# Optimization experiments

Hardware: AMD Instinct MI355X
Metric: run time of the kernel (lower is better)

The kernel has to match this reference:

```python
import jax, jax.numpy as jnp
import numpy as np

HIDDEN = 1024
HEADS = 16
HEAD_DIM = HIDDEN // HEADS


def setup_inputs() -> dict:
    key = jax.random.key(0)
    k_x, k_wq, k_bq, k_wo, k_bo = jax.random.split(key, 5)
    x = jax.random.normal(k_x, (2, 2048, HIDDEN), dtype=jnp.float32)
    s = 1.0 / np.sqrt(HIDDEN)
    W_qkv = jax.random.uniform(k_wq, (HIDDEN, 3 * HIDDEN), jnp.float32, -s, s)
    b_qkv = jax.random.uniform(k_bq, (3 * HIDDEN,), jnp.float32, -s, s)
    W_out = jax.random.uniform(k_wo, (HIDDEN, HIDDEN), jnp.float32, -s, s)
    b_out = jax.random.uniform(k_bo, (HIDDEN,), jnp.float32, -s, s)
    return {"x": x, "W_qkv": W_qkv, "b_qkv": b_qkv, "W_out": W_out, "b_out": b_out}


def reference(x, W_qkv, b_qkv, W_out, b_out):
    B, S, D = x.shape
    qkv = x @ W_qkv + b_qkv                       # [B,S,3D]
    qkv = qkv.reshape(B, S, 3, HEADS, HEAD_DIM)
    qkv = jnp.transpose(qkv, (2, 0, 3, 1, 4))     # [3,B,H,S,Dh]
    q, k, v = qkv[0], qkv[1], qkv[2]
    scores = jnp.einsum("bhsd,bhtd->bhst", q, k) / np.sqrt(HEAD_DIM)
    attn = jax.nn.softmax(scores, axis=-1)        # [B,H,S,S]
    out = jnp.einsum("bhst,bhtd->bhsd", attn, v)  # [B,H,S,Dh]
    out = jnp.transpose(out, (0, 2, 1, 3)).reshape(B, S, D)
    return out @ W_out + b_out
```

## Files before the change

### kernel.cpp

```cpp
#include <hip/hip_runtime.h>
#include <hip/hip_bf16.h>

typedef short short8 __attribute__((ext_vector_type(8)));
typedef float float4_ __attribute__((ext_vector_type(4)));
typedef unsigned short ushort_t;
typedef unsigned int uint32_t_;
typedef uint32_t_ uint2v __attribute__((ext_vector_type(2)));
typedef uint32_t_ uint4v __attribute__((ext_vector_type(4)));

#define SCL 0.1803368801111f

__device__ __forceinline__ ushort_t f2bf(float f) {
    uint32_t_ u = __builtin_bit_cast(uint32_t_, f);
    u = (u + 0x7fffu + ((u >> 16) & 1u)) >> 16;
    return (ushort_t)u;
}

__device__ __forceinline__ uint32_t_ pack_bf16(float a, float b) {
    uint32_t_ ua = __builtin_bit_cast(uint32_t_, a) + 0x8000u;
    uint32_t_ ub = __builtin_bit_cast(uint32_t_, b) + 0x8000u;
    return __builtin_amdgcn_perm(ub, ua, 0x07060302);
}

__device__ __forceinline__ uint32_t_ cvt_pk_bf16(float lo, float hi) {
    uint32_t_ r;
    asm("v_cvt_pk_bf16_f32 %0, %1, %2" : "=v"(r) : "v"(lo), "v"(hi));
    return r;
}

#define MFMA32(a, b, c) __builtin_amdgcn_mfma_f32_16x16x32_bf16(a, b, c, 0, 0, 0)

#define GLD_LDS16(g, l) __builtin_amdgcn_global_load_lds( \
    (const __attribute__((address_space(1))) void*)(g),   \
    (__attribute__((address_space(3))) void*)(l), 16, 0, 0)

__global__ __launch_bounds__(256)
void prep_k(const float* __restrict__ x, ushort_t* __restrict__ x_bf,
            const float* __restrict__ Wqkv, ushort_t* __restrict__ WqkvT,
            const float* __restrict__ Wout, ushort_t* __restrict__ WoutT) {
    __shared__ float tile[32][33];
    const int id = blockIdx.x;
    const int tid = threadIdx.x;
    if (id < 4096) {
        int i = (id * 256 + tid) * 4;
        float4 v = *(const float4*)(x + i);
        uint32_t_ lo = (uint32_t_)f2bf(v.x) | ((uint32_t_)f2bf(v.y) << 16);
        uint32_t_ hi = (uint32_t_)f2bf(v.z) | ((uint32_t_)f2bf(v.w) << 16);
        *(uint2*)(x_bf + i) = make_uint2(lo, hi);
        return;
    }
    const float* in;
    ushort_t* out;
    int N, K, n0, k0;
    if (id < 7168) {
        int t = id - 4096;
        in = Wqkv; out = WqkvT; N = 3072; K = 1024;
        n0 = (t % 96) * 32; k0 = (t / 96) * 32;
    } else {
        int t = id - 7168;
        in = Wout; out = WoutT; N = 1024; K = 1024;
        n0 = (t & 31) * 32; k0 = (t >> 5) * 32;
    }
    int tx = tid & 31, ty = tid >> 5;
    #pragma unroll
    for (int i = 0; i < 32; i += 8)
        tile[ty + i][tx] = in[(size_t)(k0 + ty + i) * N + n0 + tx];
    __syncthreads();
    #pragma unroll
    for (int i = 0; i < 32; i += 8)
        out[(size_t)(n0 + ty + i) * K + k0 + tx] = f2bf(tile[tx][ty + i]);
}

template <int TN, bool QKV_EPI>
__global__ __launch_bounds__(256, TN == 128 ? 3 : 4)
void gemm_dbuf_k(const ushort_t* __restrict__ A, const ushort_t* __restrict__ Bt,
                 const float* __restrict__ bias, void* __restrict__ C,
                 ushort_t* __restrict__ Vt_out, int M, int N, int K) {
    constexpr int NB   = TN / 32;
    constexpr int SETB = 8192 + TN * 64;
    __shared__ char smem[2 * SETB];
    const int tid  = threadIdx.x;
    const int nwg = gridDim.x * gridDim.y;
    const int id  = blockIdx.y * gridDim.x + blockIdx.x;
    const int sid = (id & 7) * (nwg >> 3) + (id >> 3);
    const int m0  = (sid / gridDim.x) * 128;
    const int n0  = (sid % gridDim.x) * TN;
    const int w    = tid >> 6;
    const int lane = tid & 63;
    const int wm   = (w >> 1) * 64;
    const int wn   = (w & 1) * (TN / 2);
    const int quad = lane >> 4;
    const int l16  = lane & 15;

    const int sr = 16 * w + (lane >> 2);
    const int sc = ((lane & 3) ^ ((sr >> 1) & 3)) * 8;
    const ushort_t* ag0 = A  + (size_t)(m0 + sr) * K + sc;
    const ushort_t* ag1 = A  + (size_t)(m0 + sr + 64) * K + sc;
    const ushort_t* bg0 = Bt + (size_t)(n0 + sr) * K + sc;
    const ushort_t* bg1 = Bt + (size_t)(n0 + sr + 64) * K + sc;
    char* sA = smem + 1024 * w;
    char* sB = smem + 8192 + 1024 * w;

    int aoff[4], boff[NB];
    #pragma unroll
    for (int i = 0; i < 4; i++) {
        int row = wm + i * 16 + l16;
        aoff[i] = row * 64 + ((quad ^ ((row >> 1) & 3)) * 16);
    }
    #pragma unroll
    for (int i = 0; i < NB; i++) {
        int row = wn + i * 16 + l16;
        boff[i] = 8192 + row * 64 + ((quad ^ ((row >> 1) & 3)) * 16);
    }

    float4_ acc[4][NB] = {};
    const int NIT = K >> 5;

    GLD_LDS16(ag0, sA);
    GLD_LDS16(ag1, sA + 4096);
    GLD_LDS16(bg0, sB);
    if (TN == 128) GLD_LDS16(bg1, sB + 4096);

    for (int it = 0; it < NIT; ++it) {
        __syncthreads();
        if (it + 1 < NIT) {
            const int nk = (it + 1) * 32;
            char* dA = sA + ((it + 1) & 1) * SETB;
            char* dB = sB + ((it + 1) & 1) * SETB;
            GLD_LDS16(ag0 + nk, dA);
            GLD_LDS16(ag1 + nk, dA + 4096);
            GLD_LDS16(bg0 + nk, dB);
            if (TN == 128) GLD_LDS16(bg1 + nk, dB + 4096);
        }
        const char* base = smem + (it & 1) * SETB;
        short8 af[4], bf[NB];
        #pragma unroll
        for (int i = 0; i < 4; i++)  af[i] = *(const short8*)(base + aoff[i]);
        #pragma unroll
        for (int i = 0; i < NB; i++) bf[i] = *(const short8*)(base + boff[i]);
        #pragma unroll
        for (int mi = 0; mi < 4; mi++)
            #pragma unroll
            for (int ni = 0; ni < NB; ni++)
                acc[mi][ni] = MFMA32(af[mi], bf[ni], acc[mi][ni]);
    }

    #pragma unroll
    for (int mi = 0; mi < 4; mi++) {
        int row = m0 + wm + mi * 16 + quad * 4;
        #pragma unroll
        for (int ni = 0; ni < NB; ni++) {
            int col = n0 + wn + ni * 16 + l16;
            float bb = bias[col];
            if (QKV_EPI) {
                if (col < 2048) {
                    float sc2 = (col < 1024) ? SCL : 1.0f;
                    #pragma unroll
                    for (int r = 0; r < 4; r++)
                        ((ushort_t*)C)[(size_t)(row + r) * 2048 + col] =
                            f2bf((acc[mi][ni][r] + bb) * sc2);
                } else {
                    int s0v  = row & 2047;
                    int spos = (s0v & ~31) | (quad << 3) | ((mi & 1) << 2);
                    size_t vrow = (size_t)((row >> 11) * 1024 + (col - 2048));
                    float v0 = acc[mi][ni][0] + bb, v1 = acc[mi][ni][1] + bb;
                    float v2 = acc[mi][ni][2] + bb, v3 = acc[mi][ni][3] + bb;
                    uint2v pk;
                    pk.x = pack_bf16(v0, v1);
                    pk.y = pack_bf16(v2, v3);
                    *(uint2v*)(Vt_out + vrow * 2048 + spos) = pk;
                }
            } else {
                #pragma unroll
                for (int r = 0; r < 4; r++)
                    ((float*)C)[(size_t)(row + r) * N + col] = acc[mi][ni][r] + bb;
            }
        }
    }
}

__global__ __launch_bounds__(512, 4)
void flash_attn_k(const ushort_t* __restrict__ qk, const ushort_t* __restrict__ vt,
                  ushort_t* __restrict__ out) {
    __shared__ char smem[49152];
    const int bh = blockIdx.x;
    const int b  = bh >> 4, h = bh & 15;
    const int q0 = blockIdx.y * 128;
    const int tid  = threadIdx.x;
    const int w    = tid >> 6;
    const int lane = tid & 63;
    const int quad = lane >> 4;
    const int l16  = lane & 15;
    const int qh   = w >> 1;
    const int kh   = w & 1;
    const size_t tok0 = (size_t)b * 2048;
    const int hq = h * 64;

    const int s7  = lane & 7;
    const int rk  = 8 * w + (lane >> 3);
    const int ck  = (s7 ^ ((rk >> 1) & 7)) * 8;
    const int rq0 = 16 * w + (lane >> 3), rq1 = rq0 + 8;
    const int cq0 = (s7 ^ ((rq0 >> 1) & 7)) * 8;
    const int cq1 = (s7 ^ ((rq1 >> 1) & 7)) * 8;
    const ushort_t* qg0 = qk + (tok0 + q0 + rq0) * 2048 + hq + cq0;
    const ushort_t* qg1 = qk + (tok0 + q0 + rq1) * 2048 + hq + cq1;
    const ushort_t* kg  = qk + (tok0 + rk) * 2048 + 1024 + hq + ck;
    const ushort_t* vg  = vt + (size_t)(bh * 64 + rk) * 2048 + ck;
    char* stK = smem + 1024 * w;
    char* stV = smem + 8192 + 1024 * w;
    char* stQ = smem + 32768 + 2048 * w;

    GLD_LDS16(qg0, stQ);
    GLD_LDS16(qg1, stQ + 1024);
    GLD_LDS16(kg, stK);
    GLD_LDS16(vg, stV);
    __syncthreads();

    const int sw = (l16 >> 1) & 7;
    short8 qf[2][2];
    #pragma unroll
    for (int sub = 0; sub < 2; sub++)
        #pragma unroll
        for (int kk = 0; kk < 2; kk++) {
            int row = qh * 32 + sub * 16 + l16;
            qf[sub][kk] = *(const short8*)(smem + 32768 + row * 128 +
                                           (((kk * 4 + quad) ^ sw) * 16));
        }

    int koff[2][2], voff[4];
    #pragma unroll
    for (int mi = 0; mi < 2; mi++)
        #pragma unroll
        for (int kk = 0; kk < 2; kk++) {
            int row = kh * 32 + mi * 16 + l16;
            koff[mi][kk] = row * 128 + (((kk * 4 + quad) ^ sw) * 16);
        }
    #pragma unroll
    for (int di = 0; di < 4; di++) {
        int row = di * 16 + l16;
        voff[di] = 8192 + row * 128 + (((kh * 4 + quad) ^ sw) * 16);
    }

    float4_ ot[2][4] = {};
    float lsum[2] = {0.f, 0.f};
    short8 vprev[4];
    short8 bpprev[2];

    const ushort_t* kp = kg + (size_t)64 * 2048;
    const ushort_t* vp = vg + 64;

    {
        __syncthreads();
        GLD_LDS16(kp, stK + 16384);
        GLD_LDS16(vp, stV + 16384);
        kp += (size_t)64 * 2048;
        vp += 64;
        const char* base = smem;
        float4_ st[2][2];
        #pragma unroll
        for (int mi = 0; mi < 2; mi++) {
            short8 kf0 = *(const short8*)(base + koff[mi][0]);
            short8 kf1 = *(const short8*)(base + koff[mi][1]);
            #pragma unroll
            for (int sub = 0; sub < 2; sub++) {
                float4_ z = {0.f, 0.f, 0.f, 0.f};
                z = MFMA32(kf0, qf[sub][0], z);
                z = MFMA32(kf1, qf[sub][1], z);
                st[mi][sub] = z;
            }
        }
        #pragma unroll
        for (int di = 0; di < 4; di++)
            vprev[di] = *(const short8*)(base + voff[di]);
        #pragma unroll
        for (int sub = 0; sub < 2; sub++) {
            uint4v u;
            #pragma unroll
            for (int mi = 0; mi < 2; mi++) {
                float p0 = __builtin_amdgcn_exp2f(st[mi][sub][0]);
                float p1 = __builtin_amdgcn_exp2f(st[mi][sub][1]);
                float p2 = __builtin_amdgcn_exp2f(st[mi][sub][2]);
                float p3 = __builtin_amdgcn_exp2f(st[mi][sub][3]);
                lsum[sub] += (p0 + p1) + (p2 + p3);
                if (mi == 0) { u.x = cvt_pk_bf16(p0, p1); u.y = cvt_pk_bf16(p2, p3); }
                else         { u.z = cvt_pk_bf16(p0, p1); u.w = cvt_pk_bf16(p2, p3); }
            }
            bpprev[sub] = __builtin_bit_cast(short8, u);
        }
    }

    for (int kt = 64; kt < 2048; kt += 64) {
        __syncthreads();
        const int set = (kt >> 6) & 1;
        if (kt + 64 < 2048) {
            const int nb = (set ^ 1) * 16384;
            GLD_LDS16(kp, stK + nb);
            GLD_LDS16(vp, stV + nb);
            kp += (size_t)64 * 2048;
            vp += 64;
        }
        const char* base = smem + set * 16384;

        float4_ st[2][2];
        #pragma unroll
        for (int mi = 0; mi < 2; mi++) {
            short8 kf0 = *(const short8*)(base + koff[mi][0]);
            short8 kf1 = *(const short8*)(base + koff[mi][1]);
            #pragma unroll
            for (int sub = 0; sub < 2; sub++) {
                float4_ z = {0.f, 0.f, 0.f, 0.f};
                z = MFMA32(kf0, qf[sub][0], z);
                z = MFMA32(kf1, qf[sub][1], z);
                st[mi][sub] = z;
            }
        }

        #pragma unroll
        for (int di = 0; di < 4; di++)
            #pragma unroll
            for (int sub = 0; sub < 2; sub++)
                ot[sub][di] = MFMA32(vprev[di], bpprev[sub], ot[sub][di]);

        #pragma unroll
        for (int di = 0; di < 4; di++)
            vprev[di] = *(const short8*)(base + voff[di]);

        #pragma unroll
        for (int sub = 0; sub < 2; sub++) {
            uint4v u;
            #pragma unroll
            for (int mi = 0; mi < 2; mi++) {
                float p0 = __builtin_amdgcn_exp2f(st[mi][sub][0]);
                float p1 = __builtin_amdgcn_exp2f(st[mi][sub][1]);
                float p2 = __builtin_amdgcn_exp2f(st[mi][sub][2]);
                float p3 = __builtin_amdgcn_exp2f(st[mi][sub][3]);
                lsum[sub] += (p0 + p1) + (p2 + p3);
                if (mi == 0) { u.x = cvt_pk_bf16(p0, p1); u.y = cvt_pk_bf16(p2, p3); }
                else         { u.z = cvt_pk_bf16(p0, p1); u.w = cvt_pk_bf16(p2, p3); }
            }
            bpprev[sub] = __builtin_bit_cast(short8, u);
        }
    }

    #pragma unroll
    for (int di = 0; di < 4; di++)
        #pragma unroll
        for (int sub = 0; sub < 2; sub++)
            ot[sub][di] = MFMA32(vprev[di], bpprev[sub], ot[sub][di]);

    #pragma unroll
    for (int sub = 0; sub < 2; sub++) {
        float t = lsum[sub];
        t += __shfl_xor(t, 16, 64);
        t += __shfl_xor(t, 32, 64);
        lsum[sub] = t;
    }

    float* Obuf = (float*)smem;
    float* lbuf = (float*)(smem + 34816);
    __syncthreads();
    #pragma unroll
    for (int sub = 0; sub < 2; sub++)
        lbuf[(qh * 32 + sub * 16 + l16) * 2 + kh] = lsum[sub];
    if (kh == 1) {
        #pragma unroll
        for (int sub = 0; sub < 2; sub++)
            #pragma unroll
            for (int di = 0; di < 4; di++)
                *(float4_*)&Obuf[(qh * 32 + sub * 16 + l16) * 68 + di * 16 + quad * 4] = ot[sub][di];
    }
    __syncthreads();
    if (kh == 0) {
        #pragma unroll
        for (int sub = 0; sub < 2; sub++)
            #pragma unroll
            for (int di = 0; di < 4; di++) {
                float4_* p = (float4_*)&Obuf[(qh * 32 + sub * 16 + l16) * 68 + di * 16 + quad * 4];
                *p = *p + ot[sub][di];
            }
    }
    __syncthreads();

    {
        int q  = tid >> 2;
        int ds = (tid & 3) * 16;
        float linv = 1.0f / (lbuf[q * 2] + lbuf[q * 2 + 1]);
        const float* ob = &Obuf[q * 68 + ds];
        float4_ v0 = *(const float4_*)(ob);
        float4_ v1 = *(const float4_*)(ob + 4);
        float4_ v2 = *(const float4_*)(ob + 8);
        float4_ v3 = *(const float4_*)(ob + 12);
        uint4v d0, d1;
        d0.x = pack_bf16(v0[0] * linv, v0[1] * linv);
        d0.y = pack_bf16(v0[2] * linv, v0[3] * linv);
        d0.z = pack_bf16(v1[0] * linv, v1[1] * linv);
        d0.w = pack_bf16(v1[2] * linv, v1[3] * linv);
        d1.x = pack_bf16(v2[0] * linv, v2[1] * linv);
        d1.y = pack_bf16(v2[2] * linv, v2[3] * linv);
        d1.z = pack_bf16(v3[0] * linv, v3[1] * linv);
        d1.w = pack_bf16(v3[2] * linv, v3[3] * linv);
        ushort_t* dst = out + (tok0 + q0 + (size_t)q) * 1024 + hq + ds;
        *(uint4v*)(dst)     = d0;
        *(uint4v*)(dst + 8) = d1;
    }
}

extern "C" void kernel_launch(void* const* d_in, const int* in_sizes, int n_in,
                              void* d_out, int out_size, void* d_ws, size_t ws_size,
                              hipStream_t stream) {
    const float* x    = (const float*)d_in[0];
    const float* Wqkv = (const float*)d_in[1];
    const float* bqkv = (const float*)d_in[2];
    const float* Wout = (const float*)d_in[3];
    const float* bout = (const float*)d_in[4];
    float* out = (float*)d_out;

    char* ws = (char*)d_ws;
    ushort_t* x_bf    = (ushort_t*)(ws);
    ushort_t* WqkvT   = (ushort_t*)(ws + 8388608);
    ushort_t* WoutT   = (ushort_t*)(ws + 14680064);
    ushort_t* qk_bf   = (ushort_t*)(ws + 16777216);
    ushort_t* vt_bf   = (ushort_t*)(ws + 33554432);
    ushort_t* attn_bf = (ushort_t*)(ws + 41943040);

    prep_k<<<8192, 256, 0, stream>>>(x, x_bf, Wqkv, WqkvT, Wout, WoutT);

    gemm_dbuf_k<128, true><<<dim3(24, 32), 256, 0, stream>>>(
        x_bf, WqkvT, bqkv, (void*)qk_bf, vt_bf, 4096, 3072, 1024);

    flash_attn_k<<<dim3(32, 16), 512, 0, stream>>>(qk_bf, vt_bf, attn_bf);

    gemm_dbuf_k<64, false><<<dim3(16, 32), 256, 0, stream>>>(
        attn_bf, WoutT, bout, (void*)out, nullptr, 4096, 1024, 1024);
}
```

Baseline: 174.1 us.

## Fuse fp32-to-bf16 conversion of x into the QKV GEMM A-tile loads

Removes the separate x conversion pass from the prep kernel. The QKV GEMM now reads fp32 x directly. It prefetches the next A tile into registers, converts it with v_cvt_pk_bf16 after the MFMAs, and stores it into the LDS double buffer. This avoids writing and re-reading a bf16 copy of x. In exchange, the GEMM reads twice the A bytes across all column blocks and stages A through registers instead of direct global-to-LDS loads, which raises register pressure.

```diff
diff --git a/kernel.cpp b/kernel.cpp
--- a/kernel.cpp
+++ b/kernel.cpp
@@ -35,29 +35,19 @@
     (__attribute__((address_space(3))) void*)(l), 16, 0, 0)
 
 __global__ __launch_bounds__(256)
-void prep_k(const float* __restrict__ x, ushort_t* __restrict__ x_bf,
-            const float* __restrict__ Wqkv, ushort_t* __restrict__ WqkvT,
+void prep_k(const float* __restrict__ Wqkv, ushort_t* __restrict__ WqkvT,
             const float* __restrict__ Wout, ushort_t* __restrict__ WoutT) {
     __shared__ float tile[32][33];
     const int id = blockIdx.x;
     const int tid = threadIdx.x;
-    if (id < 4096) {
-        int i = (id * 256 + tid) * 4;
-        float4 v = *(const float4*)(x + i);
-        uint32_t_ lo = (uint32_t_)f2bf(v.x) | ((uint32_t_)f2bf(v.y) << 16);
-        uint32_t_ hi = (uint32_t_)f2bf(v.z) | ((uint32_t_)f2bf(v.w) << 16);
-        *(uint2*)(x_bf + i) = make_uint2(lo, hi);
-        return;
-    }
     const float* in;
     ushort_t* out;
     int N, K, n0, k0;
-    if (id < 7168) {
-        int t = id - 4096;
+    if (id < 3072) {
         in = Wqkv; out = WqkvT; N = 3072; K = 1024;
-        n0 = (t % 96) * 32; k0 = (t / 96) * 32;
+        n0 = (id % 96) * 32; k0 = (id / 96) * 32;
     } else {
-        int t = id - 7168;
+        int t = id - 3072;
         in = Wout; out = WoutT; N = 1024; K = 1024;
         n0 = (t & 31) * 32; k0 = (t >> 5) * 32;
     }
@@ -71,9 +61,9 @@
         out[(size_t)(n0 + ty + i) * K + k0 + tx] = f2bf(tile[tx][ty + i]);
 }
 
-template <int TN, bool QKV_EPI>
+template <int TN, bool QKV_EPI, bool AF32>
 __global__ __launch_bounds__(256, TN == 128 ? 3 : 4)
-void gemm_dbuf_k(const ushort_t* __restrict__ A, const ushort_t* __restrict__ Bt,
+void gemm_dbuf_k(const void* __restrict__ Aptr, const ushort_t* __restrict__ Bt,
                  const float* __restrict__ bias, void* __restrict__ C,
                  ushort_t* __restrict__ Vt_out, int M, int N, int K) {
     constexpr int NB   = TN / 32;
@@ -94,8 +84,17 @@
 
     const int sr = 16 * w + (lane >> 2);
     const int sc = ((lane & 3) ^ ((sr >> 1) & 3)) * 8;
-    const ushort_t* ag0 = A  + (size_t)(m0 + sr) * K + sc;
-    const ushort_t* ag1 = A  + (size_t)(m0 + sr + 64) * K + sc;
+    const ushort_t* ag0;
+    const ushort_t* ag1;
+    const float* agf0;
+    const float* agf1;
+    if constexpr (AF32) {
+        agf0 = (const float*)Aptr + (size_t)(m0 + sr) * K + sc;
+        agf1 = agf0 + (size_t)64 * K;
+    } else {
+        ag0 = (const ushort_t*)Aptr + (size_t)(m0 + sr) * K + sc;
+        ag1 = ag0 + (size_t)64 * K;
+    }
     const ushort_t* bg0 = Bt + (size_t)(n0 + sr) * K + sc;
     const ushort_t* bg1 = Bt + (size_t)(n0 + sr + 64) * K + sc;
     char* sA = smem + 1024 * w;
@@ -116,19 +115,42 @@
     float4_ acc[4][NB] = {};
     const int NIT = K >> 5;
 
-    GLD_LDS16(ag0, sA);
-    GLD_LDS16(ag1, sA + 4096);
+    if constexpr (AF32) {
+        float4 a = *(const float4*)(agf0);
+        float4 b = *(const float4*)(agf0 + 4);
+        float4 c = *(const float4*)(agf1);
+        float4 d = *(const float4*)(agf1 + 4);
+        uint4v p, q;
+        p.x = cvt_pk_bf16(a.x, a.y); p.y = cvt_pk_bf16(a.z, a.w);
+        p.z = cvt_pk_bf16(b.x, b.y); p.w = cvt_pk_bf16(b.z, b.w);
+        q.x = cvt_pk_bf16(c.x, c.y); q.y = cvt_pk_bf16(c.z, c.w);
+        q.z = cvt_pk_bf16(d.x, d.y); q.w = cvt_pk_bf16(d.z, d.w);
+        *(uint4v*)(sA + lane * 16) = p;
+        *(uint4v*)(sA + 4096 + lane * 16) = q;
+    } else {
+        GLD_LDS16(ag0, sA);
+        GLD_LDS16(ag1, sA + 4096);
+    }
     GLD_LDS16(bg0, sB);
     if (TN == 128) GLD_LDS16(bg1, sB + 4096);
 
     for (int it = 0; it < NIT; ++it) {
         __syncthreads();
-        if (it + 1 < NIT) {
-            const int nk = (it + 1) * 32;
-            char* dA = sA + ((it + 1) & 1) * SETB;
-            char* dB = sB + ((it + 1) & 1) * SETB;
-            GLD_LDS16(ag0 + nk, dA);
-            GLD_LDS16(ag1 + nk, dA + 4096);
+        const bool pf = (it + 1 < NIT);
+        const int nk = (it + 1) * 32;
+        char* dA = sA + ((it + 1) & 1) * SETB;
+        char* dB = sB + ((it + 1) & 1) * SETB;
+        float4 a, b, c, d;
+        if (pf) {
+            if constexpr (AF32) {
+                a = *(const float4*)(agf0 + nk);
+                b = *(const float4*)(agf0 + nk + 4);
+                c = *(const float4*)(agf1 + nk);
+                d = *(const float4*)(agf1 + nk + 4);
+            } else {
+                GLD_LDS16(ag0 + nk, dA);
+                GLD_LDS16(ag1 + nk, dA + 4096);
+            }
             GLD_LDS16(bg0 + nk, dB);
             if (TN == 128) GLD_LDS16(bg1 + nk, dB + 4096);
         }
@@ -143,6 +165,17 @@
             #pragma unroll
             for (int ni = 0; ni < NB; ni++)
                 acc[mi][ni] = MFMA32(af[mi], bf[ni], acc[mi][ni]);
+        if constexpr (AF32) {
+            if (pf) {
+                uint4v p, q;
+                p.x = cvt_pk_bf16(a.x, a.y); p.y = cvt_pk_bf16(a.z, a.w);
+                p.z = cvt_pk_bf16(b.x, b.y); p.w = cvt_pk_bf16(b.z, b.w);
+                q.x = cvt_pk_bf16(c.x, c.y); q.y = cvt_pk_bf16(c.z, c.w);
+                q.z = cvt_pk_bf16(d.x, d.y); q.w = cvt_pk_bf16(d.z, d.w);
+                *(uint4v*)(dA + lane * 16) = p;
+                *(uint4v*)(dA + 4096 + lane * 16) = q;
+            }
+        }
     }
 
     #pragma unroll
@@ -416,20 +449,19 @@
     float* out = (float*)d_out;
 
     char* ws = (char*)d_ws;
-    ushort_t* x_bf    = (ushort_t*)(ws);
     ushort_t* WqkvT   = (ushort_t*)(ws + 8388608);
     ushort_t* WoutT   = (ushort_t*)(ws + 14680064);
     ushort_t* qk_bf   = (ushort_t*)(ws + 16777216);
     ushort_t* vt_bf   = (ushort_t*)(ws + 33554432);
     ushort_t* attn_bf = (ushort_t*)(ws + 41943040);
 
-    prep_k<<<8192, 256, 0, stream>>>(x, x_bf, Wqkv, WqkvT, Wout, WoutT);
-
-    gemm_dbuf_k<128, true><<<dim3(24, 32), 256, 0, stream>>>(
-        x_bf, WqkvT, bqkv, (void*)qk_bf, vt_bf, 4096, 3072, 1024);
+    prep_k<<<4096, 256, 0, stream>>>(Wqkv, WqkvT, Wout, WoutT);
+
+    gemm_dbuf_k<128, true, true><<<dim3(24, 32), 256, 0, stream>>>(
+        (const void*)x, WqkvT, bqkv, (void*)qk_bf, vt_bf, 4096, 3072, 1024);
 
     flash_attn_k<<<dim3(32, 16), 512, 0, stream>>>(qk_bf, vt_bf, attn_bf);
 
-    gemm_dbuf_k<64, false><<<dim3(16, 32), 256, 0, stream>>>(
-        attn_bf, WoutT, bout, (void*)out, nullptr, 4096, 1024, 1024);
-}
+    gemm_dbuf_k<64, false, false><<<dim3(16, 32), 256, 0, stream>>>(
+        (const void*)attn_bf, WoutT, bout, (void*)out, nullptr, 4096, 1024, 1024);
+}
```

New measurement: 184.8 us. +6.1%, slower.
